# Kernel optimization log

Measured on AMD Instinct MI355X. Metric: run time of the kernel, lower is better.

The kernel has to match this reference:

```python
import jax, jax.numpy as jnp
import numpy as np

B, S = 256, 32          # sequence layout for the final (b, s, 1) reshape
BATCH = B * S           # 8192 flattened rows processed per call
IN, U, OUT = 32, 128, 1 # sensory inputs, interneurons, motor outputs
UNFOLDS = 6             # semi-implicit ODE solver unfolds


def _syn_sigmoid(v, mu, sigma):
    # v: [B, P]; mu, sigma: [P, Q] -> [B, P, Q] per-synapse gate
    return jax.nn.sigmoid(sigma * (v[:, :, None] - mu))


def setup_inputs() -> dict:
    key = jax.random.key(0)
    ks = jax.random.split(key, 12)
    inputs = jax.random.normal(ks[0], (BATCH, IN), dtype=jnp.float32)
    state = jax.random.normal(ks[1], (BATCH, U), dtype=jnp.float32)
    # adjacency in {-1, 0, 1} (wiring polarity), baked into W / erev as in _get_variables
    sens_adj = jax.random.randint(ks[2], (IN, U), -1, 2).astype(jnp.float32)
    adj = jax.random.randint(ks[3], (U, U), -1, 2).astype(jnp.float32)
    sensory_mu = jax.random.uniform(ks[4], (IN, U)) * 0.5 + 0.3
    sensory_sigma = jax.random.uniform(ks[5], (IN, U)) * 5.0 + 3.0
    # NOTE: original applies +w_init_min OUTSIDE the |adj| mask; reproduced faithfully
    sensory_W = jnp.abs(sens_adj) * jax.random.uniform(ks[6], (IN, U)) * 0.9 + 0.1
    sensory_erev = sens_adj  # erev_init_factor = 1
    mu = jax.random.uniform(ks[7], (U, U)) * 0.5 + 0.3
    sigma = jax.random.uniform(ks[8], (U, U)) * 5.0 + 3.0
    W = jnp.abs(adj) * jax.random.uniform(ks[9], (U, U)) * 0.9 + 0.1
    erev = adj
    vleak = jax.random.uniform(ks[10], (U,)) * 0.4 - 0.2
    gleak = jnp.ones((U,), jnp.float32)        # gleak_init_min == gleak_init_max == 1
    cm_t = jnp.ones((U,), jnp.float32) * 0.5    # cm_init_min == cm_init_max == 0.5
    in_w = jnp.ones((IN,), jnp.float32)         # affine input mapping (init ones/zeros)
    in_b = jnp.zeros((IN,), jnp.float32)
    out_w = jnp.ones((OUT,), jnp.float32)       # affine output mapping
    out_b = jnp.zeros((OUT,), jnp.float32)
    return dict(inputs=inputs, state=state, sensory_mu=sensory_mu,
                sensory_sigma=sensory_sigma, sensory_W=sensory_W,
                sensory_erev=sensory_erev, mu=mu, sigma=sigma, W=W, erev=erev,
                vleak=vleak, gleak=gleak, cm_t=cm_t, in_w=in_w, in_b=in_b,
                out_w=out_w, out_b=out_b, b=B, s=S)


def reference(inputs, state, sensory_mu, sensory_sigma, sensory_W, sensory_erev,
              mu, sigma, W, erev, vleak, gleak, cm_t, in_w, in_b, out_w, out_b,
              b, s):
    x = inputs * in_w + in_b                                   # _map_inputs (Affine)
    # sensory synapse activations, computed once: [BATCH, IN, U]
    sa = sensory_W * _syn_sigmoid(x, sensory_mu, sensory_sigma)
    w_num_s = jnp.sum(sa * sensory_erev, axis=1)               # [BATCH, U]
    w_den_s = jnp.sum(sa, axis=1)                              # [BATCH, U]

    def step(v, _):
        wa = W * _syn_sigmoid(v, mu, sigma)                    # [BATCH, U, U]
        w_num = jnp.sum(wa * erev, axis=1) + w_num_s
        w_den = jnp.sum(wa, axis=1) + w_den_s
        v_new = (cm_t * v + gleak * vleak + w_num) / (cm_t + gleak + w_den)
        return v_new, None

    v, _ = jax.lax.scan(step, state, None, length=UNFOLDS)
    outputs = (v[:, :OUT] * out_w + out_b).reshape(b, s, 1)    # _map_outputs
    return outputs, v
```

## Files before the change

kernel.cpp:

```cpp
#include <hip/hip_runtime.h>

#define NIN 32
#define NU  128
#define RPB 4
#define NQ  4
#define UNFOLDS 6
#define LOG2E 1.44269504088896340736f

typedef float float4v __attribute__((ext_vector_type(4)));

#define SPN (NIN * NU)
#define RPN (NU * NU)

__global__ void pack_params(const float* __restrict__ mu,
                            const float* __restrict__ sig,
                            const float* __restrict__ W,
                            const float* __restrict__ erev,
                            float4v* __restrict__ out, int n) {
    int idx = blockIdx.x * blockDim.x + threadIdx.x;
    if (idx < n) {
        float sg = sig[idx];
        float s2 = -LOG2E * sg;
        float sm2 = -s2 * mu[idx];
        float Wv = W[idx];
        float We = Wv * erev[idx];
        out[idx] = (float4v){s2, sm2, We, Wv};
    }
}

#define EVAL_PAIR(p, v0, v1, n0, d0, n1, d1)                                   \
    {                                                                          \
        float e0 = __builtin_amdgcn_exp2f(__builtin_fmaf((p).x, (v0), (p).y)); \
        float e1 = __builtin_amdgcn_exp2f(__builtin_fmaf((p).x, (v1), (p).y)); \
        float a1 = 1.0f + e1;                                                  \
        float P  = __builtin_fmaf(e0, a1, a1);                                 \
        float rq = __builtin_amdgcn_rcpf(P);                                   \
        float s0 = rq * a1;                                                    \
        float s1 = __builtin_fmaf(rq, e0, rq);                                 \
        (n0) = __builtin_fmaf((p).z, s0, (n0));                                \
        (d0) = __builtin_fmaf((p).w, s0, (d0));                                \
        (n1) = __builtin_fmaf((p).z, s1, (n1));                                \
        (d1) = __builtin_fmaf((p).w, s1, (d1));                                \
    }

__global__ __launch_bounds__(512, 8)
void wormnet_main(const float* __restrict__ inputs,
                  const float* __restrict__ state,
                  const float4v* __restrict__ sp,
                  const float4v* __restrict__ rp,
                  const float* __restrict__ vleak,
                  const float* __restrict__ gleak,
                  const float* __restrict__ cm_t,
                  const float* __restrict__ in_w, const float* __restrict__ in_b,
                  const float* __restrict__ out_w, const float* __restrict__ out_b,
                  float* __restrict__ out_y,
                  float* __restrict__ out_v)
{
    __shared__ __align__(16) float xs[NIN * RPB];
    __shared__ __align__(16) float vs[NU * RPB];
    __shared__ float rn[RPB][NQ][NU];
    __shared__ float rd[RPB][NQ][NU];

    const int tid  = threadIdx.x;
    const int j    = tid & (NU - 1);
    const int q    = tid >> 7;
    const int base = blockIdx.x * RPB;

    if (tid < NIN * RPB) {
        int i = tid & (NIN - 1);
        int r = tid >> 5;
        xs[i * RPB + r] = inputs[(base + r) * NIN + i] * in_w[i] + in_b[i];
    }
    float vold = state[(base + q) * NU + j];
    vs[j * RPB + q] = vold;
    __syncthreads();

    float numS[RPB], denS[RPB];
    #pragma unroll
    for (int r = 0; r < RPB; ++r) { numS[r] = 0.0f; denS[r] = 0.0f; }
    {
        const float4v* pp = sp + q * (NIN / NQ) * NU + j;
        #pragma unroll 4
        for (int ii = 0; ii < NIN / NQ; ++ii) {
            const int i = q * (NIN / NQ) + ii;
            float4v p = pp[0]; pp += NU;
            float4v xv = *(const float4v*)&xs[i * RPB];
            EVAL_PAIR(p, xv[0], xv[1], numS[0], denS[0], numS[1], denS[1]);
            EVAL_PAIR(p, xv[2], xv[3], numS[2], denS[2], numS[3], denS[3]);
        }
    }

    const float cm = cm_t[j];
    const float gl = gleak[j];
    const float glvl = gl * vleak[j];
    const float cg = cm + gl;

    for (int u = 0; u < UNFOLDS; ++u) {
        float num[RPB], den[RPB];
        #pragma unroll
        for (int r = 0; r < RPB; ++r) { num[r] = numS[r]; den[r] = denS[r]; }

        const float4v* pp = rp + q * (NU / NQ) * NU + j;
        #pragma unroll 4
        for (int ii = 0; ii < NU / NQ; ++ii) {
            const int i = q * (NU / NQ) + ii;
            float4v p = pp[0]; pp += NU;
            float4v vv = *(const float4v*)&vs[i * RPB];
            EVAL_PAIR(p, vv[0], vv[1], num[0], den[0], num[1], den[1]);
            EVAL_PAIR(p, vv[2], vv[3], num[2], den[2], num[3], den[3]);
        }

        #pragma unroll
        for (int r = 0; r < RPB; ++r) {
            rn[r][q][j] = num[r];
            rd[r][q][j] = den[r];
        }
        __syncthreads();

        {
            float tn = (rn[q][0][j] + rn[q][1][j]) + (rn[q][2][j] + rn[q][3][j]);
            float td = (rd[q][0][j] + rd[q][1][j]) + (rd[q][2][j] + rd[q][3][j]);
            float vn = (__builtin_fmaf(cm, vold, glvl) + tn)
                       * __builtin_amdgcn_rcpf(cg + td);
            vold = vn;
            vs[j * RPB + q] = vn;
        }
        __syncthreads();
    }

    out_v[(base + q) * NU + j] = vold;
    if (j == 0) {
        out_y[base + q] = __builtin_fmaf(vold, out_w[0], out_b[0]);
    }
}

extern "C" void kernel_launch(void* const* d_in, const int* in_sizes, int n_in,
                              void* d_out, int out_size, void* d_ws, size_t ws_size,
                              hipStream_t stream) {
    const float* inputs  = (const float*)d_in[0];
    const float* state   = (const float*)d_in[1];
    const float* smu     = (const float*)d_in[2];
    const float* ssig    = (const float*)d_in[3];
    const float* sW      = (const float*)d_in[4];
    const float* serev   = (const float*)d_in[5];
    const float* rmu     = (const float*)d_in[6];
    const float* rsig    = (const float*)d_in[7];
    const float* rW      = (const float*)d_in[8];
    const float* rerev   = (const float*)d_in[9];
    const float* vleak   = (const float*)d_in[10];
    const float* gleak   = (const float*)d_in[11];
    const float* cm_t    = (const float*)d_in[12];
    const float* in_w    = (const float*)d_in[13];
    const float* in_b    = (const float*)d_in[14];
    const float* out_w   = (const float*)d_in[15];
    const float* out_b   = (const float*)d_in[16];

    const int batch = in_sizes[1] / NU;
    float* out_y = (float*)d_out;
    float* out_v = (float*)d_out + batch;

    float4v* sp = (float4v*)d_ws;
    float4v* rp = sp + SPN;

    hipLaunchKernelGGL(pack_params, dim3((SPN + 255) / 256), dim3(256), 0, stream,
                       smu, ssig, sW, serev, sp, SPN);
    hipLaunchKernelGGL(pack_params, dim3((RPN + 255) / 256), dim3(256), 0, stream,
                       rmu, rsig, rW, rerev, rp, RPN);

    dim3 grid(batch / RPB), block(NU * NQ);
    hipLaunchKernelGGL(wormnet_main, grid, block, 0, stream,
                       inputs, state, sp, rp,
                       vleak, gleak, cm_t, in_w, in_b, out_w, out_b,
                       out_y, out_v);
}
```

Baseline: 274.7 us.

## Split synapse sigmoid work between exp/rcp path and LDS lookup table

Adds a per-block 4096-entry sigmoid lookup table in shared memory and a second packed parameter set pre-scaled for table indexing. Two of the four thread groups keep the exact exp/rcp pair evaluation, while the other two use clamped table lookups. Row ranges are redistributed unevenly so the table-based groups handle more rows. The aim is to offload the transcendental unit onto LDS reads, at the cost of quantized sigmoid accuracy, extra LDS use that may reduce occupancy, and possible bank conflicts on gather reads.

```diff
diff --git a/kernel.cpp b/kernel.cpp
--- a/kernel.cpp
+++ b/kernel.cpp
@@ -6,17 +6,24 @@
 #define NQ  4
 #define UNFOLDS 6
 #define LOG2E 1.44269504088896340736f
+#define TBL_N 4096
+#define TBL_SCALE 128.0f
+#define TBL_OFF 2048.5f
 
 typedef float float4v __attribute__((ext_vector_type(4)));
 
 #define SPN (NIN * NU)
 #define RPN (NU * NU)
+
+__device__ __constant__ int RLOC[5] = {0, 18, 36, 82, 128};
+__device__ __constant__ int SLOC[5] = {0, 4, 8, 20, 32};
 
 __global__ void pack_params(const float* __restrict__ mu,
                             const float* __restrict__ sig,
                             const float* __restrict__ W,
                             const float* __restrict__ erev,
-                            float4v* __restrict__ out, int n) {
+                            float4v* __restrict__ out_e,
+                            float4v* __restrict__ out_t, int n) {
     int idx = blockIdx.x * blockDim.x + threadIdx.x;
     if (idx < n) {
         float sg = sig[idx];
@@ -24,7 +31,9 @@
         float sm2 = -s2 * mu[idx];
         float Wv = W[idx];
         float We = Wv * erev[idx];
-        out[idx] = (float4v){s2, sm2, We, Wv};
+        out_e[idx] = (float4v){s2, sm2, We, Wv};
+        out_t[idx] = (float4v){TBL_SCALE * s2,
+                               __builtin_fmaf(TBL_SCALE, sm2, TBL_OFF), We, Wv};
     }
 }
 
@@ -43,11 +52,20 @@
         (d1) = __builtin_fmaf((p).w, s1, (d1));                                \
     }
 
+#define EVAL_TBL(p, v, n_, d_)                                                 \
+    {                                                                          \
+        float af = __builtin_fmaf((p).x, (v), (p).y);                          \
+        af = __builtin_amdgcn_fmed3f(af, 0.0f, (float)(TBL_N - 1));            \
+        float s = tbl[(unsigned)af];                                           \
+        (n_) = __builtin_fmaf((p).z, s, (n_));                                 \
+        (d_) = __builtin_fmaf((p).w, s, (d_));                                 \
+    }
+
 __global__ __launch_bounds__(512, 8)
 void wormnet_main(const float* __restrict__ inputs,
                   const float* __restrict__ state,
-                  const float4v* __restrict__ sp,
-                  const float4v* __restrict__ rp,
+                  const float4v* __restrict__ spe, const float4v* __restrict__ spt,
+                  const float4v* __restrict__ rpe, const float4v* __restrict__ rpt,
                   const float* __restrict__ vleak,
                   const float* __restrict__ gleak,
                   const float* __restrict__ cm_t,
@@ -56,6 +74,7 @@
                   float* __restrict__ out_y,
                   float* __restrict__ out_v)
 {
+    __shared__ __align__(16) float tbl[TBL_N];
     __shared__ __align__(16) float xs[NIN * RPB];
     __shared__ __align__(16) float vs[NU * RPB];
     __shared__ float rn[RPB][NQ][NU];
@@ -66,6 +85,12 @@
     const int q    = tid >> 7;
     const int base = blockIdx.x * RPB;
 
+    #pragma unroll
+    for (int k = tid; k < TBL_N; k += 512) {
+        float t = (float)(k - TBL_N / 2) * (1.0f / TBL_SCALE);
+        tbl[k] = __builtin_amdgcn_rcpf(1.0f + __builtin_amdgcn_exp2f(t));
+    }
+
     if (tid < NIN * RPB) {
         int i = tid & (NIN - 1);
         int r = tid >> 5;
@@ -75,19 +100,30 @@
     vs[j * RPB + q] = vold;
     __syncthreads();
 
+    const int slo = SLOC[q], shi = SLOC[q + 1];
+    const int rlo = RLOC[q], rhi = RLOC[q + 1];
+
     float numS[RPB], denS[RPB];
     #pragma unroll
     for (int r = 0; r < RPB; ++r) { numS[r] = 0.0f; denS[r] = 0.0f; }
-    {
-        const float4v* pp = sp + q * (NIN / NQ) * NU + j;
-        #pragma unroll 4
-        for (int ii = 0; ii < NIN / NQ; ++ii) {
-            const int i = q * (NIN / NQ) + ii;
+    if (q < 2) {
+        const float4v* pp = spe + slo * NU + j;
+        #pragma unroll 2
+        for (int i = slo; i < shi; ++i) {
             float4v p = pp[0]; pp += NU;
             float4v xv = *(const float4v*)&xs[i * RPB];
             EVAL_PAIR(p, xv[0], xv[1], numS[0], denS[0], numS[1], denS[1]);
             EVAL_PAIR(p, xv[2], xv[3], numS[2], denS[2], numS[3], denS[3]);
         }
+    } else {
+        const float4v* pp = spt + slo * NU + j;
+        #pragma unroll 2
+        for (int i = slo; i < shi; ++i) {
+            float4v p = pp[0]; pp += NU;
+            float4v xv = *(const float4v*)&xs[i * RPB];
+            #pragma unroll
+            for (int r = 0; r < RPB; ++r) { EVAL_TBL(p, xv[r], numS[r], denS[r]); }
+        }
     }
 
     const float cm = cm_t[j];
@@ -100,14 +136,24 @@
         #pragma unroll
         for (int r = 0; r < RPB; ++r) { num[r] = numS[r]; den[r] = denS[r]; }
 
-        const float4v* pp = rp + q * (NU / NQ) * NU + j;
-        #pragma unroll 4
-        for (int ii = 0; ii < NU / NQ; ++ii) {
-            const int i = q * (NU / NQ) + ii;
-            float4v p = pp[0]; pp += NU;
-            float4v vv = *(const float4v*)&vs[i * RPB];
-            EVAL_PAIR(p, vv[0], vv[1], num[0], den[0], num[1], den[1]);
-            EVAL_PAIR(p, vv[2], vv[3], num[2], den[2], num[3], den[3]);
+        if (q < 2) {
+            const float4v* pp = rpe + rlo * NU + j;
+            #pragma unroll 2
+            for (int i = rlo; i < rhi; ++i) {
+                float4v p = pp[0]; pp += NU;
+                float4v vv = *(const float4v*)&vs[i * RPB];
+                EVAL_PAIR(p, vv[0], vv[1], num[0], den[0], num[1], den[1]);
+                EVAL_PAIR(p, vv[2], vv[3], num[2], den[2], num[3], den[3]);
+            }
+        } else {
+            const float4v* pp = rpt + rlo * NU + j;
+            #pragma unroll 2
+            for (int i = rlo; i < rhi; ++i) {
+                float4v p = pp[0]; pp += NU;
+                float4v vv = *(const float4v*)&vs[i * RPB];
+                #pragma unroll
+                for (int r = 0; r < RPB; ++r) { EVAL_TBL(p, vv[r], num[r], den[r]); }
+            }
         }
 
         #pragma unroll
@@ -159,17 +205,19 @@
     float* out_y = (float*)d_out;
     float* out_v = (float*)d_out + batch;
 
-    float4v* sp = (float4v*)d_ws;
-    float4v* rp = sp + SPN;
+    float4v* spe = (float4v*)d_ws;
+    float4v* spt = spe + SPN;
+    float4v* rpe = spt + SPN;
+    float4v* rpt = rpe + RPN;
 
     hipLaunchKernelGGL(pack_params, dim3((SPN + 255) / 256), dim3(256), 0, stream,
-                       smu, ssig, sW, serev, sp, SPN);
+                       smu, ssig, sW, serev, spe, spt, SPN);
     hipLaunchKernelGGL(pack_params, dim3((RPN + 255) / 256), dim3(256), 0, stream,
-                       rmu, rsig, rW, rerev, rp, RPN);
+                       rmu, rsig, rW, rerev, rpe, rpt, RPN);
 
     dim3 grid(batch / RPB), block(NU * NQ);
     hipLaunchKernelGGL(wormnet_main, grid, block, 0, stream,
-                       inputs, state, sp, rp,
+                       inputs, state, spe, spt, rpe, rpt,
                        vleak, gleak, cm_t, in_w, in_b, out_w, out_b,
                        out_y, out_v);
 }
```

Result: faster. 266.5 us (-3.0%).
